# Kernel optimization log

Measured on AMD Instinct MI355X. Metric: run time of the kernel, lower is better.

Reference implementation:

```python
import jax, jax.numpy as jnp
import numpy as np

B, T, C = 4, 2048, 1024
NH = 16
HD = C // NH  # 64

def setup_inputs() -> dict:
    key = jax.random.key(0)
    k1, k2, k3 = jax.random.split(key, 3)
    x = jax.random.normal(k1, (B, T, C), dtype=jnp.float32)
    w_qkv = jax.random.normal(k2, (C, 3 * C), dtype=jnp.float32) * (1.0 / np.sqrt(C))
    w_out = jax.random.normal(k3, (C, C), dtype=jnp.float32) * (1.0 / np.sqrt(C))
    b_out = jnp.zeros((C,), dtype=jnp.float32)
    return {"x": x, "w_qkv": w_qkv, "w_out": w_out, "b_out": b_out}

def reference(x, w_qkv, w_out, b_out):
    b, t, c = x.shape
    nh, hd = NH, c // NH
    qkv = x @ w_qkv                      # [b, t, 3c]
    q, k, v = jnp.split(qkv, 3, axis=-1)
    # [b, t, c] -> [b, nh, t, hd]
    def heads(z):
        return z.reshape(b, t, nh, hd).transpose(0, 2, 1, 3)
    q, k, v = heads(q), heads(k), heads(v)
    scale = 1.0 / jnp.sqrt(jnp.asarray(hd, dtype=x.dtype))
    scores = jnp.einsum('bhqd,bhkd->bhqk', q, k) * scale  # [b, nh, t, t]
    causal = jnp.tril(jnp.ones((t, t), dtype=bool))
    scores = jnp.where(causal, scores, jnp.asarray(-jnp.inf, dtype=scores.dtype))
    attn = jax.nn.softmax(scores, axis=-1)
    ctx = jnp.einsum('bhqk,bhkd->bhqd', attn, v)           # [b, nh, t, hd]
    ctx = ctx.transpose(0, 2, 1, 3).reshape(b, t, c)
    return ctx @ w_out + b_out
```

## Files before the change

kernel.cpp:

```cpp
#include <hip/hip_runtime.h>
#include <cmath>


typedef __bf16 bf16x4 __attribute__((ext_vector_type(4)));
typedef __bf16 bf16x8 __attribute__((ext_vector_type(8)));
typedef float  f32x4  __attribute__((ext_vector_type(4)));
typedef float  f32x16 __attribute__((ext_vector_type(16)));

__device__ __forceinline__ void gload_lds16(const __bf16* g, __bf16* l) {
    __builtin_amdgcn_global_load_lds(
        (const __attribute__((address_space(1))) void*)g,
        (__attribute__((address_space(3))) void*)l,
        16, 0, 0);
}

__device__ __forceinline__ unsigned packbf(float a, float b) {
    union { __bf16 h[2]; unsigned u; } t;
    t.h[0] = (__bf16)a; t.h[1] = (__bf16)b;
    return t.u;
}

__device__ __forceinline__ void permswap(unsigned& a, unsigned& b) {
    asm volatile("v_permlane32_swap_b32 %0, %1" : "+v"(a), "+v"(b));
}

#define BAR()  __builtin_amdgcn_s_barrier()
#define VM2()  { asm volatile("s_waitcnt vmcnt(2)" ::: "memory"); \
                 __builtin_amdgcn_sched_barrier(0); }

__global__ __launch_bounds__(256) void cast_bf16(const float* __restrict__ in,
                                                 __bf16* __restrict__ out, int n4) {
    int i = blockIdx.x * 256 + threadIdx.x;
    if (i >= n4) return;
    float4 f = *(const float4*)(in + (size_t)i * 4);
    bf16x4 o;
    o[0] = (__bf16)f.x; o[1] = (__bf16)f.y; o[2] = (__bf16)f.z; o[3] = (__bf16)f.w;
    *(bf16x4*)(out + (size_t)i * 4) = o;
}

__global__ __launch_bounds__(256) void transpose_cast(const float* __restrict__ W,
                                                      __bf16* __restrict__ WT,
                                                      int K, int N) {
    __shared__ float tile[32][33];
    const int n0 = blockIdx.x * 32, k0 = blockIdx.y * 32;
    const int tx = threadIdx.x & 31, ty = threadIdx.x >> 5;
    #pragma unroll
    for (int i = 0; i < 4; ++i)
        tile[ty + 8 * i][tx] = W[(size_t)(k0 + ty + 8 * i) * N + n0 + tx];
    __syncthreads();
    #pragma unroll
    for (int i = 0; i < 4; ++i)
        WT[(size_t)(n0 + ty + 8 * i) * K + k0 + tx] = (__bf16)tile[tx][ty + 8 * i];
}

__global__ __launch_bounds__(256) void transpose_v(const __bf16* __restrict__ qkv,
                                                   __bf16* __restrict__ Vt) {
    constexpr int T = 2048, R3C = 3072;
    __shared__ __bf16 tile[64][72];
    const int bh = blockIdx.y;
    const int b  = bh >> 4, h = bh & 15;
    const int kt = blockIdx.x * 64;
    const int tid = threadIdx.x;
    #pragma unroll
    for (int i = 0; i < 2; ++i) {
        int idx = tid + 256 * i;
        int kr  = idx >> 3;
        int c8  = idx & 7;
        *(uint4*)&tile[kr][c8 * 8] =
            *(const uint4*)(qkv + (size_t)(b * T + kt + kr) * R3C + 2048 + h * 64 + c8 * 8);
    }
    __syncthreads();
    #pragma unroll
    for (int i = 0; i < 2; ++i) {
        int idx = tid + 256 * i;
        int d   = idx >> 3;
        int k8  = idx & 7;
        union { __bf16 v[8]; uint4 u; } t;
        #pragma unroll
        for (int j = 0; j < 8; ++j) t.v[j] = tile[k8 * 8 + j][d];
        *(uint4*)(Vt + ((size_t)bh * 64 + d) * T + kt + k8 * 8) = t.u;
    }
}

__global__ __launch_bounds__(512) void gemm256(const __bf16* __restrict__ A,
                                               const __bf16* __restrict__ BT,
                                               __bf16* __restrict__ Cc,
                                               int M, int N, int K) {
    __shared__ __attribute__((aligned(16))) char lds[98304];
    const int tid = threadIdx.x, lane = tid & 63, w = tid >> 6;
    const int wr = w >> 1, wc = w & 1, cc = lane & 15, gg = lane >> 4;

    const int cpx = gridDim.x >> 3;
    const int swz = ((int)blockIdx.x & 7) * cpx + ((int)blockIdx.x >> 3);
    const int nbx = N >> 7;
    const int rowBase = (swz / nbx) << 8;
    const int colBase = (swz % nbx) << 7;
    const int NT = K >> 6;

    const int sChunk = (lane & 7) ^ (((lane >> 5) & 1) << 1);
    const int rsub   = lane >> 3;

    auto stA = [&](int t, int h) {
        const int buf = t & 1, k0 = (t % NT) * 64;
        #pragma unroll
        for (int l = 0; l < 2; ++l) {
            int idx   = l * 8 + w;
            int rbase = h * 128 + idx * 8;
            gload_lds16(A + (size_t)(rowBase + rbase + rsub) * K + k0 + sChunk * 8,
                        (__bf16*)(lds + buf * 32768 + rbase * 128 + lane * 16));
        }
    };
    auto stB = [&](int t) {
        const int buf = t & 1, k0 = (t % NT) * 64;
        #pragma unroll
        for (int l = 0; l < 2; ++l) {
            int idx   = l * 8 + w;
            int rbase = idx * 8;
            gload_lds16(BT + (size_t)(colBase + rbase + rsub) * K + k0 + sChunk * 8,
                        (__bf16*)(lds + 65536 + buf * 16384 + rbase * 128 + lane * 16));
        }
    };

    f32x4 acc[4][4];
    #pragma unroll
    for (int i = 0; i < 4; ++i)
        #pragma unroll
        for (int j = 0; j < 4; ++j) acc[i][j] = f32x4{0.f, 0.f, 0.f, 0.f};
    bf16x8 afr[4], bfr[8];

    auto rdA = [&](int buf, int mh) {
        const char* base = lds + buf * 32768;
        #pragma unroll
        for (int i = 0; i < 2; ++i)
            #pragma unroll
            for (int kk = 0; kk < 2; ++kk) {
                int r  = wr * 64 + mh * 32 + i * 16 + cc;
                int cb = (kk * 64 + gg * 16) ^ (((cc >> 2) & 1) << 5);
                afr[i * 2 + kk] = *(const bf16x8*)(base + r * 128 + cb);
            }
    };
    auto rdB = [&](int buf) {
        const char* base = lds + 65536 + buf * 16384;
        #pragma unroll
        for (int j = 0; j < 4; ++j)
            #pragma unroll
            for (int kk = 0; kk < 2; ++kk) {
                int r  = wc * 64 + j * 16 + cc;
                int cb = (kk * 64 + gg * 16) ^ (((cc >> 2) & 1) << 5);
                bfr[j * 2 + kk] = *(const bf16x8*)(base + r * 128 + cb);
            }
    };

#define QMFMA(MH, NH)                                                        \
    _Pragma("unroll") for (int i = 0; i < 2; ++i)                            \
    _Pragma("unroll") for (int j = 0; j < 2; ++j)                            \
    _Pragma("unroll") for (int kk = 0; kk < 2; ++kk)                         \
        acc[(MH)*2 + i][(NH)*2 + j] = __builtin_amdgcn_mfma_f32_16x16x32_bf16( \
            afr[i*2 + kk], bfr[((NH)*2 + j)*2 + kk], acc[(MH)*2 + i][(NH)*2 + j], 0, 0, 0);

    stA(0, 0); stB(0); stA(0, 1); stB(1);
    VM2(); BAR();

    for (int t = 0; t < NT; ++t) {
        const int buf = t & 1;
        rdA(buf, 0); rdB(buf);
        stA(t + 1, 0);
        BAR();
        __builtin_amdgcn_s_setprio(1); QMFMA(0, 0); __builtin_amdgcn_s_setprio(0);
        BAR();
        stA(t + 1, 1);
        BAR();
        __builtin_amdgcn_s_setprio(1); QMFMA(0, 1); __builtin_amdgcn_s_setprio(0);
        BAR();
        rdA(buf, 1);
        stB(t + 2);
        BAR();
        __builtin_amdgcn_s_setprio(1); QMFMA(1, 0); __builtin_amdgcn_s_setprio(0);
        BAR();
        BAR();
        __builtin_amdgcn_s_setprio(1); QMFMA(1, 1); __builtin_amdgcn_s_setprio(0);
        VM2(); BAR();
    }
#undef QMFMA

    #pragma unroll
    for (int i = 0; i < 4; ++i)
        #pragma unroll
        for (int j = 0; j < 4; ++j) {
            const int col = colBase + wc * 64 + j * 16 + cc;
            #pragma unroll
            for (int rr = 0; rr < 4; ++rr) {
                const int row = rowBase + wr * 64 + i * 16 + gg * 4 + rr;
                Cc[(size_t)row * N + col] = (__bf16)acc[i][j][rr];
            }
        }
}

template <typename OutT, bool BIAS>
__global__ __launch_bounds__(256) void gemm_bt(const __bf16* __restrict__ A,
                                               const __bf16* __restrict__ BT,
                                               OutT* __restrict__ Cc,
                                               const float* __restrict__ bias,
                                               int M, int N, int K) {
    __shared__ __bf16 As[128 * 32];
    __shared__ __bf16 Bs[128 * 32];

    const int tid  = threadIdx.x;
    const int lane = tid & 63;
    const int w    = tid >> 6;
    const int wr   = w >> 1, wc = w & 1;
    const int cc   = lane & 15, gg = lane >> 4;
    const int rowBase = blockIdx.y * 128;
    const int colBase = blockIdx.x * 128;

    f32x4 acc[4][4];
    #pragma unroll
    for (int i = 0; i < 4; ++i)
        #pragma unroll
        for (int j = 0; j < 4; ++j) acc[i][j] = f32x4{0.f, 0.f, 0.f, 0.f};

    for (int k0 = 0; k0 < K; k0 += 32) {
        __syncthreads();
        #pragma unroll
        for (int i = 0; i < 2; ++i) {
            int idx = tid + 256 * i;
            int r   = idx >> 2;
            int c4  = idx & 3;
            gload_lds16(A  + (size_t)(rowBase + r) * K + k0 + c4 * 8, &As[idx * 8]);
            gload_lds16(BT + (size_t)(colBase + r) * K + k0 + c4 * 8, &Bs[idx * 8]);
        }
        __syncthreads();

        bf16x8 af[4], bfr2[4];
        #pragma unroll
        for (int i = 0; i < 4; ++i)
            af[i] = *(const bf16x8*)&As[(wr * 64 + i * 16 + cc) * 32 + gg * 8];
        #pragma unroll
        for (int j = 0; j < 4; ++j)
            bfr2[j] = *(const bf16x8*)&Bs[(wc * 64 + j * 16 + cc) * 32 + gg * 8];
        #pragma unroll
        for (int i = 0; i < 4; ++i)
            #pragma unroll
            for (int j = 0; j < 4; ++j)
                acc[i][j] = __builtin_amdgcn_mfma_f32_16x16x32_bf16(af[i], bfr2[j], acc[i][j], 0, 0, 0);
    }

    #pragma unroll
    for (int i = 0; i < 4; ++i)
        #pragma unroll
        for (int j = 0; j < 4; ++j) {
            const int col = colBase + wc * 64 + j * 16 + cc;
            #pragma unroll
            for (int r = 0; r < 4; ++r) {
                const int row = rowBase + wr * 64 + i * 16 + gg * 4 + r;
                float v = acc[i][j][r];
                if (BIAS) v += bias[col];
                Cc[(size_t)row * N + col] = (OutT)v;
            }
        }
}

__global__ __launch_bounds__(256) void flash_attn_mfma(const __bf16* __restrict__ qkv,
                                                       const __bf16* __restrict__ Vt,
                                                       __bf16* __restrict__ ctx) {
    constexpr int T = 2048, C = 1024, HD = 64;
    constexpr int R3C = 3 * C;
    constexpr float K1 = 0.125f * 1.44269504088896f;
    constexpr float K2 = -16.0f * 1.44269504088896f;

    const int tid  = threadIdx.x;
    const int lane = tid & 63;
    const int w    = tid >> 6;
    const int q5   = lane & 31;
    const int half = lane >> 5;

    const int bh   = blockIdx.x;
    const int y    = blockIdx.y;
    const int qtA  = 15 - y;
    const int qtB  = y;
    const int b    = bh >> 4;
    const int h    = bh & 15;
    const int srowA = qtA * 128 + w * 32;
    const int srowB = qtB * 128 + w * 32;
    const int ktmaxA = qtA * 128 + 64;
    const int ktmaxB = qtB * 128 + 64;

    __shared__ __attribute__((aligned(16))) __bf16 KsL[2][64][64];
    __shared__ __attribute__((aligned(16))) __bf16 VsL[2][64][64];

    const __bf16* QrowA = qkv + (size_t)(b * T + srowA + q5) * R3C + h * HD;
    const __bf16* QrowB = qkv + (size_t)(b * T + srowB + q5) * R3C + h * HD;
    bf16x8 QbA[4], QbB[4];
    #pragma unroll
    for (int ks = 0; ks < 4; ++ks) {
        QbA[ks] = *(const bf16x8*)(QrowA + ks * 16 + half * 8);
        QbB[ks] = *(const bf16x8*)(QrowB + ks * 16 + half * 8);
    }

    f32x16 OA[2], OB[2];
    #pragma unroll
    for (int mb = 0; mb < 2; ++mb)
        #pragma unroll
        for (int r = 0; r < 16; ++r) { OA[mb][r] = 0.f; OB[mb][r] = 0.f; }
    float lsumA = 0.f, lsumB = 0.f;

    const __bf16* Kb  = qkv + (size_t)(b * T) * R3C + C + h * HD;
    const __bf16* Vtb = Vt + (size_t)bh * 64 * T;

    auto stage = [&](int bufi, int kt) {
        #pragma unroll
        for (int i = 0; i < 2; ++i) {
            int idx = tid + 256 * i;
            int kr  = idx >> 3;
            int c8  = idx & 7;
            int cs  = c8 ^ (kr & 7);
            gload_lds16(Kb + (size_t)(kt + kr) * R3C + cs * 8,
                        &KsL[bufi][kr][c8 * 8]);
        }
        #pragma unroll
        for (int i = 0; i < 2; ++i) {
            int idx = tid + 256 * i;
            int d   = idx >> 3;
            int k8  = idx & 7;
            int ks_ = k8 ^ (d & 7);
            gload_lds16(Vtb + (size_t)d * T + kt + ks_ * 8,
                        &VsL[bufi][d][k8 * 8]);
        }
    };

    stage(0, 0);
    __syncthreads();

    for (int kt = 0; kt <= ktmaxA; kt += 64) {
        const int cur = (kt >> 6) & 1;
        if (kt + 64 <= ktmaxA) stage(cur ^ 1, kt + 64);

        const char* kbase = (const char*)KsL[cur];
        const char* vbase = (const char*)VsL[cur];

        auto subtile = [&](int sub, const bf16x8* Qb, int srow, f32x16* O, float& lsum) {
            f32x16 S;
            #pragma unroll
            for (int r = 0; r < 16; ++r) S[r] = 0.f;
            const int krow = sub * 32 + q5;
            const int kxor = (krow & 7) << 4;
            #pragma unroll
            for (int ks = 0; ks < 4; ++ks) {
                bf16x8 kb = *(const bf16x8*)(kbase + krow * 128 +
                                             (((ks * 16 + half * 8) * 2) ^ kxor));
                S = __builtin_amdgcn_mfma_f32_32x32x16_bf16(kb, Qb[ks], S, 0, 0, 0);
            }
            if (kt + sub * 32 + 31 > srow) {
                #pragma unroll
                for (int r = 0; r < 16; ++r) {
                    int key = kt + sub * 32 + (r & 3) + 8 * (r >> 2) + 4 * half;
                    if (key > srow + q5) S[r] = -1e30f;
                }
            }
            float p[16];
            #pragma unroll
            for (int r = 0; r < 16; ++r) {
                p[r] = exp2f(fmaf(S[r], K1, K2));
                lsum += p[r];
            }
            unsigned w0 = packbf(p[0],  p[1]);
            unsigned w1 = packbf(p[2],  p[3]);
            unsigned w2 = packbf(p[4],  p[5]);
            unsigned w3 = packbf(p[6],  p[7]);
            permswap(w0, w2);
            permswap(w1, w3);
            unsigned w4 = packbf(p[8],  p[9]);
            unsigned w5 = packbf(p[10], p[11]);
            unsigned w6 = packbf(p[12], p[13]);
            unsigned w7 = packbf(p[14], p[15]);
            permswap(w4, w6);
            permswap(w5, w7);
            union { unsigned u[4]; bf16x8 v; } pf0, pf1;
            pf0.u[0] = w0; pf0.u[1] = w1; pf0.u[2] = w2; pf0.u[3] = w3;
            pf1.u[0] = w4; pf1.u[1] = w5; pf1.u[2] = w6; pf1.u[3] = w7;
            const int vc = sub * 32 + half * 8;
            #pragma unroll
            for (int mb = 0; mb < 2; ++mb) {
                const int vrow = mb * 32 + q5;
                const int vxor = (vrow & 7) << 4;
                bf16x8 v0 = *(const bf16x8*)(vbase + vrow * 128 + ((vc * 2) ^ vxor));
                O[mb] = __builtin_amdgcn_mfma_f32_32x32x16_bf16(v0, pf0.v, O[mb], 0, 0, 0);
                bf16x8 v1 = *(const bf16x8*)(vbase + vrow * 128 + (((vc + 16) * 2) ^ vxor));
                O[mb] = __builtin_amdgcn_mfma_f32_32x32x16_bf16(v1, pf1.v, O[mb], 0, 0, 0);
            }
        };

        #pragma unroll
        for (int sub = 0; sub < 2; ++sub)
            subtile(sub, QbA, srowA, OA, lsumA);
        if (kt <= ktmaxB) {
            #pragma unroll
            for (int sub = 0; sub < 2; ++sub)
                subtile(sub, QbB, srowB, OB, lsumB);
        }

        __syncthreads();
    }

    const float invA = 1.f / (lsumA + __shfl_xor(lsumA, 32));
    const float invB = 1.f / (lsumB + __shfl_xor(lsumB, 32));

    __bf16* crowA = ctx + (size_t)(b * T + srowA + q5) * C + h * HD;
    __bf16* crowB = ctx + (size_t)(b * T + srowB + q5) * C + h * HD;
    #pragma unroll
    for (int mb = 0; mb < 2; ++mb)
        #pragma unroll
        for (int a = 0; a < 4; ++a) {
            union { bf16x4 v; uint2 u; } pA, pB;
            #pragma unroll
            for (int bq = 0; bq < 4; ++bq) {
                pA.v[bq] = (__bf16)(OA[mb][4 * a + bq] * invA);
                pB.v[bq] = (__bf16)(OB[mb][4 * a + bq] * invB);
            }
            *(uint2*)(crowA + mb * 32 + 8 * a + 4 * half) = pA.u;
            *(uint2*)(crowB + mb * 32 + 8 * a + 4 * half) = pB.u;
        }
}

extern "C" void kernel_launch(void* const* d_in, const int* in_sizes, int n_in,
                              void* d_out, int out_size, void* d_ws, size_t ws_size,
                              hipStream_t stream) {
    constexpr int B = 4, T = 2048, C = 1024;
    constexpr int M = B * T;

    const float* x     = (const float*)d_in[0];
    const float* w_qkv = (const float*)d_in[1];
    const float* w_out = (const float*)d_in[2];
    const float* b_out = (const float*)d_in[3];
    float* out = (float*)d_out;

    char* ws = (char*)d_ws;
    __bf16* xb     = (__bf16*)(ws);
    __bf16* wqkvT  = (__bf16*)(ws + (16ull << 20));
    __bf16* woutT  = (__bf16*)(ws + (22ull << 20));
    __bf16* qkvb   = (__bf16*)(ws + (24ull << 20));
    __bf16* ctxb   = (__bf16*)(ws + (72ull << 20));
    __bf16* Vt     = (__bf16*)(ws + (88ull << 20));

    cast_bf16<<<(M * C / 4 + 255) / 256, 256, 0, stream>>>(x, xb, M * C / 4);
    transpose_cast<<<dim3(3 * C / 32, C / 32), 256, 0, stream>>>(w_qkv, wqkvT, C, 3 * C);
    transpose_cast<<<dim3(C / 32, C / 32), 256, 0, stream>>>(w_out, woutT, C, C);

    gemm256<<<768, 512, 0, stream>>>(xb, wqkvT, qkvb, M, 3 * C, C);

    transpose_v<<<dim3(T / 64, B * 16), 256, 0, stream>>>(qkvb, Vt);

    flash_attn_mfma<<<dim3(B * 16, 8), 256, 0, stream>>>(qkvb, Vt, ctxb);

    gemm_bt<float, true><<<dim3(C / 128, M / 128), 256, 0, stream>>>(
        ctxb, woutT, out, b_out, M, C, C);
}
```

Baseline: 287.4 us.

## Reuse pipelined 256x128 GEMM for output projection and delay attention prefetch

The bf16/no-bias GEMM kernel becomes a template with optional float output and bias. The output projection now uses it with 256 blocks, replacing the simpler 128x128 single-buffered gemm_bt, which should give better LDS pipelining and MFMA scheduling. Separately, the flash attention kernel issues the next K/V tile prefetch after the first subtile instead of at the top of the iteration. This spreads memory issue among compute, at the risk of less prefetch lead time. The output GEMM grid now gives only 256 blocks for 256 CUs, so occupancy may be low.

New measurement: 279.0 us. -2.9%, faster.

```diff
diff --git a/kernel.cpp b/kernel.cpp
--- a/kernel.cpp
+++ b/kernel.cpp
@@ -82,9 +82,11 @@
     }
 }
 
+template <typename OutT, bool BIAS>
 __global__ __launch_bounds__(512) void gemm256(const __bf16* __restrict__ A,
                                                const __bf16* __restrict__ BT,
-                                               __bf16* __restrict__ Cc,
+                                               OutT* __restrict__ Cc,
+                                               const float* __restrict__ bias,
                                                int M, int N, int K) {
     __shared__ __attribute__((aligned(16))) char lds[98304];
     const int tid = threadIdx.x, lane = tid & 63, w = tid >> 6;
@@ -191,69 +193,7 @@
             #pragma unroll
             for (int rr = 0; rr < 4; ++rr) {
                 const int row = rowBase + wr * 64 + i * 16 + gg * 4 + rr;
-                Cc[(size_t)row * N + col] = (__bf16)acc[i][j][rr];
-            }
-        }
-}
-
-template <typename OutT, bool BIAS>
-__global__ __launch_bounds__(256) void gemm_bt(const __bf16* __restrict__ A,
-                                               const __bf16* __restrict__ BT,
-                                               OutT* __restrict__ Cc,
-                                               const float* __restrict__ bias,
-                                               int M, int N, int K) {
-    __shared__ __bf16 As[128 * 32];
-    __shared__ __bf16 Bs[128 * 32];
-
-    const int tid  = threadIdx.x;
-    const int lane = tid & 63;
-    const int w    = tid >> 6;
-    const int wr   = w >> 1, wc = w & 1;
-    const int cc   = lane & 15, gg = lane >> 4;
-    const int rowBase = blockIdx.y * 128;
-    const int colBase = blockIdx.x * 128;
-
-    f32x4 acc[4][4];
-    #pragma unroll
-    for (int i = 0; i < 4; ++i)
-        #pragma unroll
-        for (int j = 0; j < 4; ++j) acc[i][j] = f32x4{0.f, 0.f, 0.f, 0.f};
-
-    for (int k0 = 0; k0 < K; k0 += 32) {
-        __syncthreads();
-        #pragma unroll
-        for (int i = 0; i < 2; ++i) {
-            int idx = tid + 256 * i;
-            int r   = idx >> 2;
-            int c4  = idx & 3;
-            gload_lds16(A  + (size_t)(rowBase + r) * K + k0 + c4 * 8, &As[idx * 8]);
-            gload_lds16(BT + (size_t)(colBase + r) * K + k0 + c4 * 8, &Bs[idx * 8]);
-        }
-        __syncthreads();
-
-        bf16x8 af[4], bfr2[4];
-        #pragma unroll
-        for (int i = 0; i < 4; ++i)
-            af[i] = *(const bf16x8*)&As[(wr * 64 + i * 16 + cc) * 32 + gg * 8];
-        #pragma unroll
-        for (int j = 0; j < 4; ++j)
-            bfr2[j] = *(const bf16x8*)&Bs[(wc * 64 + j * 16 + cc) * 32 + gg * 8];
-        #pragma unroll
-        for (int i = 0; i < 4; ++i)
-            #pragma unroll
-            for (int j = 0; j < 4; ++j)
-                acc[i][j] = __builtin_amdgcn_mfma_f32_16x16x32_bf16(af[i], bfr2[j], acc[i][j], 0, 0, 0);
-    }
-
-    #pragma unroll
-    for (int i = 0; i < 4; ++i)
-        #pragma unroll
-        for (int j = 0; j < 4; ++j) {
-            const int col = colBase + wc * 64 + j * 16 + cc;
-            #pragma unroll
-            for (int r = 0; r < 4; ++r) {
-                const int row = rowBase + wr * 64 + i * 16 + gg * 4 + r;
-                float v = acc[i][j][r];
+                float v = acc[i][j][rr];
                 if (BIAS) v += bias[col];
                 Cc[(size_t)row * N + col] = (OutT)v;
             }
@@ -333,7 +273,6 @@
 
     for (int kt = 0; kt <= ktmaxA; kt += 64) {
         const int cur = (kt >> 6) & 1;
-        if (kt + 64 <= ktmaxA) stage(cur ^ 1, kt + 64);
 
         const char* kbase = (const char*)KsL[cur];
         const char* vbase = (const char*)VsL[cur];
@@ -390,13 +329,12 @@
             }
         };
 
-        #pragma unroll
-        for (int sub = 0; sub < 2; ++sub)
-            subtile(sub, QbA, srowA, OA, lsumA);
+        subtile(0, QbA, srowA, OA, lsumA);
+        if (kt + 64 <= ktmaxA) stage(cur ^ 1, kt + 64);
+        subtile(1, QbA, srowA, OA, lsumA);
         if (kt <= ktmaxB) {
-            #pragma unroll
-            for (int sub = 0; sub < 2; ++sub)
-                subtile(sub, QbB, srowB, OB, lsumB);
+            subtile(0, QbB, srowB, OB, lsumB);
+            subtile(1, QbB, srowB, OB, lsumB);
         }
 
         __syncthreads();
@@ -446,12 +384,11 @@
     transpose_cast<<<dim3(3 * C / 32, C / 32), 256, 0, stream>>>(w_qkv, wqkvT, C, 3 * C);
     transpose_cast<<<dim3(C / 32, C / 32), 256, 0, stream>>>(w_out, woutT, C, C);
 
-    gemm256<<<768, 512, 0, stream>>>(xb, wqkvT, qkvb, M, 3 * C, C);
+    gemm256<__bf16, false><<<768, 512, 0, stream>>>(xb, wqkvT, qkvb, nullptr, M, 3 * C, C);
 
     transpose_v<<<dim3(T / 64, B * 16), 256, 0, stream>>>(qkvb, Vt);
 
     flash_attn_mfma<<<dim3(B * 16, 8), 256, 0, stream>>>(qkvb, Vt, ctxb);
 
-    gemm_bt<float, true><<<dim3(C / 128, M / 128), 256, 0, stream>>>(
-        ctxb, woutT, out, b_out, M, C, C);
-}
+    gemm256<float, true><<<256, 512, 0, stream>>>(ctxb, woutT, out, b_out, M, C, C);
+}
```
